# Kernel optimization log

Measured on AMD Instinct MI355X. Metric: run time of the kernel, lower is better.

## Reference

```python
import jax, jax.numpy as jnp
import numpy as np

BITWIDTH = 8
SCALE = 2.0 ** (BITWIDTH - 1)  # bipolar SC quantization levels


def quantize(v):
    """SourceGen/BSGen over 2^bitwidth cycles converges to the bitwidth-quantized
    bipolar value in [-1, 1]; straight-through estimator keeps grads alive."""
    q = jnp.round(jnp.clip(v, -1.0, 1.0) * SCALE) / SCALE
    return v + jax.lax.stop_gradient(q - v)


def sc_clip(v):
    # non-scaled SC accumulation saturates the bipolar range [-1, 1]
    return jnp.clip(v, -1.0, 1.0)


def fsu_relu(v):
    # FSUReLU on bipolar streams: negative rates -> 0, stays in [0, 1]
    return jnp.clip(v, 0.0, 1.0)


def conv2d(x, w):
    # NCHW conv, padding=1, stride=1 (HUBConv2d / FSUConv2d rate-level math)
    return jax.lax.conv_general_dilated(
        x, w, window_strides=(1, 1), padding=[(1, 1), (1, 1)],
        dimension_numbers=("NCHW", "OIHW", "NCHW"))


def setup_inputs() -> dict:
    key = jax.random.key(0)
    ks = jax.random.split(key, 8)
    B, W, H, Wd = 2048, 10, 10, 11
    cnn_chn, fc_sz, hid, n_cls = 16, 256, 64, 7
    fc3_in = H * Wd * cnn_chn * 2  # 3520
    s = 0.1
    return {
        "x": jax.random.normal(ks[0], (B, W, H, Wd), jnp.float32) * 0.5,
        "conv1_w": jax.random.normal(ks[1], (cnn_chn, 1, 3, 3), jnp.float32) * s,
        "conv2_w": jax.random.normal(ks[2], (cnn_chn * 2, cnn_chn, 3, 3), jnp.float32) * s,
        "fc3_w": jax.random.normal(ks[3], (fc_sz, fc3_in), jnp.float32) * s,
        "w_ih": jax.random.normal(ks[4], (2 * hid, fc_sz), jnp.float32) * s,
        "w_hh": jax.random.normal(ks[5], (2 * hid, hid), jnp.float32) * s,
        "fc5_w": jax.random.normal(ks[6], (n_cls, hid), jnp.float32) * s,
    }


def _forward(x, conv1_w, conv2_w, fc3_w, w_ih, w_hh, fc5_w):
    B = x.shape[0]
    hid = w_hh.shape[1]

    def mgu_cell(x_t, hx):
        # FSUMGUCell, hard nonlinearities (rnn_hard=True)
        gi = x_t @ w_ih.T                         # [B, 2H]
        gh = hx @ w_hh.T                          # [B, 2H]
        gi_f, gi_n = jnp.split(gi, 2, axis=-1)
        gh_f, gh_n = jnp.split(gh, 2, axis=-1)
        forgetgate = jnp.clip(0.5 * (gi_f + gh_f) + 0.5, 0.0, 1.0)  # hard sigmoid
        newgate_prod = forgetgate * gh_n
        newgate = jnp.clip(gi_n + newgate_prod, -1.0, 1.0)          # hard tanh
        forgetgate_inv_prod = (1.0 - forgetgate) * newgate
        forgetgate_prod = forgetgate * hx
        return forgetgate_inv_prod + forgetgate_prod

    def step(hx, x_win):
        xi = quantize(x_win)[:, None, :, :]        # [B,1,10,11] bitstream rate
        a1 = fsu_relu(sc_clip(conv2d(xi, conv1_w)))
        a2 = fsu_relu(sc_clip(conv2d(a1, conv2_w)))
        f = a2.reshape(B, -1)                      # [B, 3520]
        a3 = fsu_relu(sc_clip(f @ fc3_w.T))        # [B, 256]
        hq = quantize(hx)
        hx_new = mgu_cell(a3, hq)
        return hx_new, None

    hx0 = jnp.zeros((B, hid), x.dtype)
    xs = jnp.transpose(x, (1, 0, 2, 3))            # [W, B, 10, 11]
    hx, _ = jax.lax.scan(step, hx0, xs)
    return hx @ fc5_w.T                            # [B, 7] fc5 logits


def reference(x, conv1_w, conv2_w, fc3_w, w_ih, w_hh, fc5_w):
    return _forward(x, conv1_w, conv2_w, fc3_w, w_ih, w_hh, fc5_w)
```

## Files before the change

### kernel.cpp

```cpp
#include <hip/hip_runtime.h>
#include <hip/hip_bf16.h>
#include <cstdint>
#include <cstddef>


typedef __bf16 bf16x8v __attribute__((ext_vector_type(8)));
typedef float  f32x4   __attribute__((ext_vector_type(4)));

#define WAVE_FENCE() asm volatile("s_waitcnt lgkmcnt(0)" ::: "memory")

#define A1_PS 24
#define A1_RS (13 * A1_PS)
#define A1_ZS (12 * A1_RS)
#define A1_BS 3776
#define XQ_RS 20
#define XQ_BS 256

#define FC3_K 3584

__global__ __launch_bounds__(256) void cvt_all_k(
    const float* __restrict__ fc3w, const float* __restrict__ w2g,
    const float* __restrict__ wih,  const float* __restrict__ whh,
    __hip_bfloat16* __restrict__ w3p, __hip_bfloat16* __restrict__ w2p,
    __hip_bfloat16* __restrict__ wfi, __hip_bfloat16* __restrict__ wfh)
{
    int bid = blockIdx.x;
    if (bid < 3584) {
        int idx = bid * 256 + threadIdx.x;
        int n = idx / FC3_K, kp = idx % FC3_K;
        int mt = kp >> 9, r = kp & 511;
        int fq = r >> 7, col = (r >> 3) & 15, nt = (r >> 2) & 1, j = r & 3;
        int pixel = mt * 16 + fq * 4 + j, oc = nt * 16 + col;
        float v = (pixel < 110) ? fc3w[n * 3520 + oc * 110 + pixel] : 0.f;
        w3p[idx] = __float2bfloat16(v);
    } else if (bid < 3604) {
        int idx = (bid - 3584) * 256 + threadIdx.x;
        if (idx < 5120) {
            int oc = idx / 160, k = idx % 160;
            int koff = k >> 4, ic = k & 15;
            float v = (koff < 9) ? w2g[(oc * 16 + ic) * 9 + koff] : 0.f;
            w2p[idx] = __float2bfloat16(v);
        }
    } else if (bid < 3860) {
        int idx = (bid - 3604) * 256 + threadIdx.x;
        int e = idx & 7, lane = (idx >> 3) & 63, hl = (idx >> 9) & 1;
        int kt = (idx >> 10) & 7, nt = (idx >> 13) & 7;
        int gate = nt * 16 + (lane & 15);
        int k = kt * 32 + (lane >> 4) * 8 + e;
        float v = wih[gate * 256 + k];
        __hip_bfloat16 hi = __float2bfloat16(v);
        wfi[idx] = hl ? __float2bfloat16(v - __bfloat162float(hi)) : hi;
    } else {
        int idx = (bid - 3860) * 256 + threadIdx.x;
        int e = idx & 7, lane = (idx >> 3) & 63, hl = (idx >> 9) & 1;
        int kt = (idx >> 10) & 1, nt = (idx >> 11) & 7;
        int gate = nt * 16 + (lane & 15);
        int k = kt * 32 + (lane >> 4) * 8 + e;
        float v = whh[gate * 64 + k];
        __hip_bfloat16 hi = __float2bfloat16(v);
        wfh[idx] = hl ? __float2bfloat16(v - __bfloat162float(hi)) : hi;
    }
}

__global__ __launch_bounds__(256) void conv_all_k(
    const float* __restrict__ x, const float* __restrict__ w1g,
    const __hip_bfloat16* __restrict__ w2p,
    __hip_bfloat16* __restrict__ a2p)
{
    __shared__ __hip_bfloat16 a1_s[4 * A1_BS];
    __shared__ float xq_s[4 * XQ_BS];

    const int tid  = threadIdx.x;
    const int wv   = tid >> 6, lane = tid & 63;
    const int t    = blockIdx.x >> 9;
    const int b    = (blockIdx.x & 511) * 4 + wv;
    const int ab   = wv * A1_BS;
    const int xb   = wv * XQ_BS;

    const int fr  = lane & 15, fq = lane >> 4;
    const int fqh = fq >> 1,  icb = (fq & 1) * 8;

    bf16x8v bfrag[5][2];
#pragma unroll
    for (int kt = 0; kt < 5; ++kt)
#pragma unroll
        for (int nt = 0; nt < 2; ++nt)
            bfrag[kt][nt] = *(const bf16x8v*)&w2p[(nt * 16 + fr) * 160 + kt * 32 + fq * 8];

    const int ocp = lane & 7, rs = lane >> 3;
    float w1a[9], w1b[9];
#pragma unroll
    for (int k = 0; k < 9; ++k) {
        w1a[k] = w1g[(2 * ocp) * 9 + k];
        w1b[k] = w1g[(2 * ocp + 1) * 9 + k];
    }

    {
        bf16x8v z = {};
#pragma unroll
        for (int i = 0; i < 8; ++i) {
            int c = lane + i * 64;
            if (c < A1_BS / 8) *(bf16x8v*)&a1_s[ab + c * 8] = z;
        }
        float4 zf = {0.f, 0.f, 0.f, 0.f};
        *(float4*)&xq_s[xb + lane * 4] = zf;
    }
    WAVE_FENCE();

#pragma unroll
    for (int pass = 0; pass < 2; ++pass) {
        int p = pass * 64 + lane;
        if (p < 110) {
            float xv = x[(size_t)b * 1100 + t * 110 + p];
            xv = fminf(fmaxf(xv, -1.f), 1.f);
            xv = rintf(xv * 128.f) * 0.0078125f;
            int h = p / 11, w = p - h * 11;
            xq_s[xb + (h + 1) * XQ_RS + (w + 1)] = xv;
        }
    }
    WAVE_FENCE();

#pragma unroll
    for (int pass = 0; pass < 2; ++pass) {
        const int hr = pass == 0 ? rs : rs + 8;
        if (hr < 10) {
            float acc0[11], acc1[11];
#pragma unroll
            for (int w = 0; w < 11; ++w) { acc0[w] = 0.f; acc1[w] = 0.f; }
#pragma unroll
            for (int dr = 0; dr < 3; ++dr) {
                float xr[16];
                const float* row = &xq_s[xb + (hr + dr) * XQ_RS];
#pragma unroll
                for (int j = 0; j < 4; ++j)
                    *(float4*)&xr[j * 4] = *(const float4*)&row[j * 4];
#pragma unroll
                for (int dc = 0; dc < 3; ++dc) {
                    float wa = w1a[dr * 3 + dc], wb = w1b[dr * 3 + dc];
#pragma unroll
                    for (int w = 0; w < 11; ++w) {
                        acc0[w] += xr[w + dc] * wa;
                        acc1[w] += xr[w + dc] * wb;
                    }
                }
            }
#pragma unroll
            for (int w = 0; w < 11; ++w) {
                __hip_bfloat162 pr;
                pr.x = __float2bfloat16(fminf(fmaxf(acc0[w], 0.f), 1.f));
                pr.y = __float2bfloat16(fminf(fmaxf(acc1[w], 0.f), 1.f));
                *(__hip_bfloat162*)&a1_s[ab + (hr + 1) * A1_RS + (w + 1) * A1_PS + 2 * ocp] = pr;
            }
        }
    }
    WAVE_FENCE();

    const int d0 = fqh * 24 + icb;
    const int d1 = (fqh ? 312 : 48) + icb;
    const int d2 = 336 + fqh * 24 + icb;
    const int d3 = 624 + fqh * 24 + icb;

#pragma unroll
    for (int m = 0; m < 7; ++m) {
        int p = m * 16 + fr; if (p > 109) p = 109;
        int h = p / 11, w = p - h * 11;
        const int bm = ab + h * A1_RS + w * A1_PS;
        f32x4 acc0 = {0.f, 0.f, 0.f, 0.f}, acc1 = {0.f, 0.f, 0.f, 0.f};
        bf16x8v a;
        a = *(const bf16x8v*)&a1_s[bm + d0];
        acc0 = __builtin_amdgcn_mfma_f32_16x16x32_bf16(a, bfrag[0][0], acc0, 0, 0, 0);
        acc1 = __builtin_amdgcn_mfma_f32_16x16x32_bf16(a, bfrag[0][1], acc1, 0, 0, 0);
        a = *(const bf16x8v*)&a1_s[bm + d1];
        acc0 = __builtin_amdgcn_mfma_f32_16x16x32_bf16(a, bfrag[1][0], acc0, 0, 0, 0);
        acc1 = __builtin_amdgcn_mfma_f32_16x16x32_bf16(a, bfrag[1][1], acc1, 0, 0, 0);
        a = *(const bf16x8v*)&a1_s[bm + d2];
        acc0 = __builtin_amdgcn_mfma_f32_16x16x32_bf16(a, bfrag[2][0], acc0, 0, 0, 0);
        acc1 = __builtin_amdgcn_mfma_f32_16x16x32_bf16(a, bfrag[2][1], acc1, 0, 0, 0);
        a = *(const bf16x8v*)&a1_s[bm + d3];
        acc0 = __builtin_amdgcn_mfma_f32_16x16x32_bf16(a, bfrag[3][0], acc0, 0, 0, 0);
        acc1 = __builtin_amdgcn_mfma_f32_16x16x32_bf16(a, bfrag[3][1], acc1, 0, 0, 0);
        a = *(const bf16x8v*)&a1_s[fqh ? (ab + A1_ZS) : (bm + 672 + icb)];
        acc0 = __builtin_amdgcn_mfma_f32_16x16x32_bf16(a, bfrag[4][0], acc0, 0, 0, 0);
        acc1 = __builtin_amdgcn_mfma_f32_16x16x32_bf16(a, bfrag[4][1], acc1, 0, 0, 0);

        bf16x8v ov;
#pragma unroll
        for (int j = 0; j < 4; ++j) {
            bool valid = (m * 16 + fq * 4 + j) < 110;
            float v0 = valid ? fminf(fmaxf(acc0[j], 0.f), 1.f) : 0.f;
            float v1 = valid ? fminf(fmaxf(acc1[j], 0.f), 1.f) : 0.f;
            ov[j]     = (__bf16)v0;
            ov[4 + j] = (__bf16)v1;
        }
        *(bf16x8v*)&a2p[(size_t)(t * 2048 + b) * FC3_K + m * 512 + lane * 8] = ov;
    }
}

__global__ __launch_bounds__(256) void fc3_all_k(
    const __hip_bfloat16* __restrict__ A,
    const __hip_bfloat16* __restrict__ W,
    __hip_bfloat16* __restrict__ a3)
{
    __shared__ __hip_bfloat16 As[3 * 128 * 64];
    __shared__ __hip_bfloat16 Bs[3 * 64 * 64];

    const int tid  = threadIdx.x;
    const int wv   = tid >> 6;
    const int lane = tid & 63;

    const int d    = blockIdx.x;
    const int xcd  = d & 7;
    const int slot = d >> 3;
    const int n0   = (slot & 3) * 64;
    const int m0   = (xcd * 20 + (slot >> 2)) * 128;

    const int wr = wv >> 1, wc = wv & 1;

    const int srow   = lane >> 3;
    const int schunk = lane & 7;
    const int swzc   = schunk ^ srow;

    const int fr = lane & 15;
    const int fq = lane >> 4;

    const __hip_bfloat16* gA0 = A + (size_t)(m0 + wv * 32 +  0 + srow) * FC3_K + swzc * 8;
    const __hip_bfloat16* gA1 = A + (size_t)(m0 + wv * 32 +  8 + srow) * FC3_K + swzc * 8;
    const __hip_bfloat16* gA2 = A + (size_t)(m0 + wv * 32 + 16 + srow) * FC3_K + swzc * 8;
    const __hip_bfloat16* gA3 = A + (size_t)(m0 + wv * 32 + 24 + srow) * FC3_K + swzc * 8;
    const __hip_bfloat16* gB0 = W + (size_t)(n0 + wv * 16 +  0 + srow) * FC3_K + swzc * 8;
    const __hip_bfloat16* gB1 = W + (size_t)(n0 + wv * 16 +  8 + srow) * FC3_K + swzc * 8;

    __hip_bfloat16* ldsA0 = &As[(wv * 32 +  0) * 64];
    __hip_bfloat16* ldsA1 = &As[(wv * 32 +  8) * 64];
    __hip_bfloat16* ldsA2 = &As[(wv * 32 + 16) * 64];
    __hip_bfloat16* ldsA3 = &As[(wv * 32 + 24) * 64];
    __hip_bfloat16* ldsB0 = &Bs[(wv * 16 +  0) * 64];
    __hip_bfloat16* ldsB1 = &Bs[(wv * 16 +  8) * 64];

#define GLD(src, dst, boff)                                                   \
    __builtin_amdgcn_global_load_lds(                                          \
        (const __attribute__((address_space(1))) void*)(src),                  \
        (__attribute__((address_space(3))) void*)((dst) + (boff)), 16, 0, 0)

#define STAGE(b)                                                               \
    do {                                                                       \
        GLD(gA0, ldsA0, (b) * 8192); GLD(gA1, ldsA1, (b) * 8192);              \
        GLD(gA2, ldsA2, (b) * 8192); GLD(gA3, ldsA3, (b) * 8192);              \
        GLD(gB0, ldsB0, (b) * 4096); GLD(gB1, ldsB1, (b) * 4096);              \
        gA0 += 64; gA1 += 64; gA2 += 64; gA3 += 64; gB0 += 64; gB1 += 64;      \
    } while (0)

    int aofs[2][4], bofs[2][2];
#pragma unroll
    for (int kk = 0; kk < 2; ++kk) {
#pragma unroll
        for (int mi = 0; mi < 4; ++mi) {
            const int rr = wr * 64 + mi * 16 + fr;
            aofs[kk][mi] = rr * 64 + (((kk * 4 + fq) ^ (rr & 7)) * 8);
        }
#pragma unroll
        for (int ni = 0; ni < 2; ++ni) {
            const int rr = wc * 32 + ni * 16 + fr;
            bofs[kk][ni] = rr * 64 + (((kk * 4 + fq) ^ (rr & 7)) * 8);
        }
    }

    f32x4 acc[4][2];
#pragma unroll
    for (int mi = 0; mi < 4; ++mi)
#pragma unroll
        for (int ni = 0; ni < 2; ++ni)
            acc[mi][ni] = (f32x4){0.f, 0.f, 0.f, 0.f};

#define COMPUTE(b)                                                             \
    do {                                                                       \
        const __hip_bfloat16* Ab = &As[(b) * 8192];                            \
        const __hip_bfloat16* Bb = &Bs[(b) * 4096];                            \
        _Pragma("unroll")                                                      \
        for (int kk = 0; kk < 2; ++kk) {                                       \
            bf16x8v af[4], bfv[2];                                             \
            _Pragma("unroll")                                                  \
            for (int mi = 0; mi < 4; ++mi)                                     \
                af[mi] = *(const bf16x8v*)&Ab[aofs[kk][mi]];                   \
            _Pragma("unroll")                                                  \
            for (int ni = 0; ni < 2; ++ni)                                     \
                bfv[ni] = *(const bf16x8v*)&Bb[bofs[kk][ni]];                  \
            _Pragma("unroll")                                                  \
            for (int mi = 0; mi < 4; ++mi)                                     \
                _Pragma("unroll")                                              \
                for (int ni = 0; ni < 2; ++ni)                                 \
                    acc[mi][ni] = __builtin_amdgcn_mfma_f32_16x16x32_bf16(     \
                        af[mi], bfv[ni], acc[mi][ni], 0, 0, 0);                \
        }                                                                      \
    } while (0)

#define WAITV(n) asm volatile("s_waitcnt vmcnt(" #n ")" ::: "memory")

    STAGE(0);
    STAGE(1);

    for (int it = 0; it < 18; ++it) {
        WAITV(6); __builtin_amdgcn_s_barrier(); COMPUTE(0); STAGE(2);
        WAITV(6); __builtin_amdgcn_s_barrier(); COMPUTE(1); STAGE(0);
        WAITV(6); __builtin_amdgcn_s_barrier(); COMPUTE(2); STAGE(1);
    }
    WAITV(6); __builtin_amdgcn_s_barrier(); COMPUTE(0);
    WAITV(0); __builtin_amdgcn_s_barrier(); COMPUTE(1);

#undef GLD
#undef STAGE
#undef COMPUTE
#undef WAITV

#pragma unroll
    for (int mi = 0; mi < 4; ++mi)
#pragma unroll
        for (int ni = 0; ni < 2; ++ni)
#pragma unroll
            for (int j = 0; j < 4; ++j) {
                int row = m0 + wr * 64 + mi * 16 + fq * 4 + j;
                int col = n0 + wc * 32 + ni * 16 + fr;
                float v = fminf(fmaxf(acc[mi][ni][j], 0.f), 1.f);
                a3[(size_t)row * 256 + col] = __float2bfloat16(v);
            }
}

__global__ __launch_bounds__(256, 1) void mgu_all_k(
    const __hip_bfloat16* __restrict__ a3,
    const __hip_bfloat16* __restrict__ wfi, const __hip_bfloat16* __restrict__ wfh,
    const float* __restrict__ w5, float* __restrict__ out)
{
    __shared__ __hip_bfloat16 a3_s[16 * 256];
    __shared__ __hip_bfloat16 hq_s[16 * 64];
    __shared__ float hx_s[16 * 64];
    __shared__ float w5_s[7 * 64];

    const int tid = threadIdx.x;
    const int wv  = tid >> 6, lane = tid & 63;
    const int fr  = lane & 15, fq = lane >> 4;
    const int b0  = blockIdx.x * 16;
    const int ntf = wv, ntn = wv + 4;

    bf16x8v wiF[8][2], wiN[8][2], whF[2][2], whN[2][2];
#pragma unroll
    for (int kt = 0; kt < 8; ++kt)
#pragma unroll
        for (int hl = 0; hl < 2; ++hl) {
            wiF[kt][hl] = *(const bf16x8v*)&wfi[(((ntf * 8 + kt) * 2 + hl) * 64 + lane) * 8];
            wiN[kt][hl] = *(const bf16x8v*)&wfi[(((ntn * 8 + kt) * 2 + hl) * 64 + lane) * 8];
        }
#pragma unroll
    for (int kt = 0; kt < 2; ++kt)
#pragma unroll
        for (int hl = 0; hl < 2; ++hl) {
            whF[kt][hl] = *(const bf16x8v*)&wfh[(((ntf * 2 + kt) * 2 + hl) * 64 + lane) * 8];
            whN[kt][hl] = *(const bf16x8v*)&wfh[(((ntn * 2 + kt) * 2 + hl) * 64 + lane) * 8];
        }

    for (int i = tid; i < 16 * 64; i += 256) hx_s[i] = 0.f;
    for (int i = tid; i < 7 * 64; i += 256) w5_s[i] = w5[i];
    __syncthreads();

    for (int t = 0; t < 10; ++t) {
#pragma unroll
        for (int pass = 0; pass < 2; ++pass) {
            int i = pass * 256 + tid;
            int r = i >> 5, cq = i & 31;
            bf16x8v v = *(const bf16x8v*)&a3[((size_t)(t * 2048 + b0 + r)) * 256 + cq * 8];
            *(bf16x8v*)&a3_s[r * 256 + ((cq ^ (r & 7)) * 8)] = v;
        }
#pragma unroll
        for (int pass = 0; pass < 4; ++pass) {
            int i = pass * 256 + tid;
            int r = i >> 6, c = i & 63;
            float v = hx_s[r * 64 + c];
            v = fminf(fmaxf(v, -1.f), 1.f);
            v = rintf(v * 128.f) * 0.0078125f;
            hq_s[r * 64 + (((c >> 3) ^ (r & 7)) << 3) + (c & 7)] = __float2bfloat16(v);
        }
        __syncthreads();

        f32x4 accF  = {0.f, 0.f, 0.f, 0.f};
        f32x4 accNi = {0.f, 0.f, 0.f, 0.f};
        f32x4 accNh = {0.f, 0.f, 0.f, 0.f};
#pragma unroll
        for (int kt = 0; kt < 8; ++kt) {
            bf16x8v a = *(const bf16x8v*)&a3_s[fr * 256 + (((kt * 4 + fq) ^ (fr & 7)) * 8)];
            accF  = __builtin_amdgcn_mfma_f32_16x16x32_bf16(a, wiF[kt][0], accF, 0, 0, 0);
            accF  = __builtin_amdgcn_mfma_f32_16x16x32_bf16(a, wiF[kt][1], accF, 0, 0, 0);
            accNi = __builtin_amdgcn_mfma_f32_16x16x32_bf16(a, wiN[kt][0], accNi, 0, 0, 0);
            accNi = __builtin_amdgcn_mfma_f32_16x16x32_bf16(a, wiN[kt][1], accNi, 0, 0, 0);
        }
#pragma unroll
        for (int kt = 0; kt < 2; ++kt) {
            bf16x8v a = *(const bf16x8v*)&hq_s[fr * 64 + (((kt * 4 + fq) ^ (fr & 7)) * 8)];
            accF  = __builtin_amdgcn_mfma_f32_16x16x32_bf16(a, whF[kt][0], accF, 0, 0, 0);
            accF  = __builtin_amdgcn_mfma_f32_16x16x32_bf16(a, whF[kt][1], accF, 0, 0, 0);
            accNh = __builtin_amdgcn_mfma_f32_16x16x32_bf16(a, whN[kt][0], accNh, 0, 0, 0);
            accNh = __builtin_amdgcn_mfma_f32_16x16x32_bf16(a, whN[kt][1], accNh, 0, 0, 0);
        }

        const int j5 = wv * 16 + fr;
#pragma unroll
        for (int j = 0; j < 4; ++j) {
            int b = fq * 4 + j;
            float f = fminf(fmaxf(0.5f * accF[j] + 0.5f, 0.f), 1.f);
            float n = fminf(fmaxf(accNi[j] + f * accNh[j], -1.f), 1.f);
            float hq = __bfloat162float(
                hq_s[b * 64 + ((((j5) >> 3) ^ (b & 7)) << 3) + (j5 & 7)]);
            hx_s[b * 64 + j5] = (1.f - f) * n + f * hq;
        }
        __syncthreads();
    }

    if (tid < 112) {
        int b = tid / 7, c = tid % 7;
        float acc = 0.f;
#pragma unroll
        for (int k = 0; k < 64; ++k) acc += hx_s[b * 64 + k] * w5_s[c * 64 + k];
        out[(size_t)(b0 + b) * 7 + c] = acc;
    }
}

extern "C" void kernel_launch(void* const* d_in, const int* in_sizes, int n_in,
                              void* d_out, int out_size, void* d_ws, size_t ws_size,
                              hipStream_t stream)
{
    const float* x    = (const float*)d_in[0];
    const float* w1   = (const float*)d_in[1];
    const float* w2   = (const float*)d_in[2];
    const float* fc3w = (const float*)d_in[3];
    const float* wih  = (const float*)d_in[4];
    const float* whh  = (const float*)d_in[5];
    const float* fc5w = (const float*)d_in[6];
    float* out = (float*)d_out;

    char* ws = (char*)d_ws;
    __hip_bfloat16* a2p = (__hip_bfloat16*)ws;
    __hip_bfloat16* a3  = (__hip_bfloat16*)(ws + 146800640);
    __hip_bfloat16* w3p = (__hip_bfloat16*)(ws + 157286400);
    __hip_bfloat16* w2p = (__hip_bfloat16*)(ws + 159121408);
    __hip_bfloat16* wfi = (__hip_bfloat16*)(ws + 159131648);
    __hip_bfloat16* wfh = (__hip_bfloat16*)(ws + 159262720);

    cvt_all_k<<<3924, 256, 0, stream>>>(fc3w, w2, wih, whh, w3p, w2p, wfi, wfh);
    conv_all_k<<<5120, 256, 0, stream>>>(x, w1, w2p, a2p);
    fc3_all_k<<<640, 256, 0, stream>>>(a2p, w3p, a3);
    mgu_all_k<<<128, 256, 0, stream>>>(a3, wfi, wfh, fc5w, out);
}
```

Measured before the change: 121.9 us.

## Restructure fc3 GEMM into single-wave 64x64 tiles without block barriers

The fc3 GEMM moves from 4-wave blocks computing 128x64 tiles with a triple-buffered LDS pipeline to 1-wave blocks computing 64x64 tiles with double buffering. Because each block is a single wave, the s_barrier calls are gone and only vmcnt waits guard the async global-to-LDS loads. s_setprio is also raised around the MFMA bursts. The aim is to cut barrier stalls and raise MFMA work per wave. In exchange the grid holds half as many waves and each block reuses less data than a 128x64 tile, so latency hiding and L2 traffic may suffer.

```diff
diff --git a/kernel.cpp b/kernel.cpp
--- a/kernel.cpp
+++ b/kernel.cpp
@@ -8,6 +8,7 @@
 typedef float  f32x4   __attribute__((ext_vector_type(4)));
 
 #define WAVE_FENCE() asm volatile("s_waitcnt lgkmcnt(0)" ::: "memory")
+#define WAITV(n) asm volatile("s_waitcnt vmcnt(" #n ")" ::: "memory")
 
 #define A1_PS 24
 #define A1_RS (13 * A1_PS)
@@ -196,25 +197,21 @@
     }
 }
 
-__global__ __launch_bounds__(256) void fc3_all_k(
+__global__ __launch_bounds__(64) void fc3_all_k(
     const __hip_bfloat16* __restrict__ A,
     const __hip_bfloat16* __restrict__ W,
     __hip_bfloat16* __restrict__ a3)
 {
-    __shared__ __hip_bfloat16 As[3 * 128 * 64];
-    __shared__ __hip_bfloat16 Bs[3 * 64 * 64];
-
-    const int tid  = threadIdx.x;
-    const int wv   = tid >> 6;
-    const int lane = tid & 63;
+    __shared__ __hip_bfloat16 As[2 * 64 * 64];
+    __shared__ __hip_bfloat16 Bs[2 * 64 * 64];
+
+    const int lane = threadIdx.x;
 
     const int d    = blockIdx.x;
     const int xcd  = d & 7;
     const int slot = d >> 3;
     const int n0   = (slot & 3) * 64;
-    const int m0   = (xcd * 20 + (slot >> 2)) * 128;
-
-    const int wr = wv >> 1, wc = wv & 1;
+    const int m0   = (xcd * 40 + (slot >> 2)) * 64;
 
     const int srow   = lane >> 3;
     const int schunk = lane & 7;
@@ -223,19 +220,22 @@
     const int fr = lane & 15;
     const int fq = lane >> 4;
 
-    const __hip_bfloat16* gA0 = A + (size_t)(m0 + wv * 32 +  0 + srow) * FC3_K + swzc * 8;
-    const __hip_bfloat16* gA1 = A + (size_t)(m0 + wv * 32 +  8 + srow) * FC3_K + swzc * 8;
-    const __hip_bfloat16* gA2 = A + (size_t)(m0 + wv * 32 + 16 + srow) * FC3_K + swzc * 8;
-    const __hip_bfloat16* gA3 = A + (size_t)(m0 + wv * 32 + 24 + srow) * FC3_K + swzc * 8;
-    const __hip_bfloat16* gB0 = W + (size_t)(n0 + wv * 16 +  0 + srow) * FC3_K + swzc * 8;
-    const __hip_bfloat16* gB1 = W + (size_t)(n0 + wv * 16 +  8 + srow) * FC3_K + swzc * 8;
-
-    __hip_bfloat16* ldsA0 = &As[(wv * 32 +  0) * 64];
-    __hip_bfloat16* ldsA1 = &As[(wv * 32 +  8) * 64];
-    __hip_bfloat16* ldsA2 = &As[(wv * 32 + 16) * 64];
-    __hip_bfloat16* ldsA3 = &As[(wv * 32 + 24) * 64];
-    __hip_bfloat16* ldsB0 = &Bs[(wv * 16 +  0) * 64];
-    __hip_bfloat16* ldsB1 = &Bs[(wv * 16 +  8) * 64];
+    const __hip_bfloat16* gA0 = A + (size_t)(m0 +  0 + srow) * FC3_K + swzc * 8;
+    const __hip_bfloat16* gA1 = A + (size_t)(m0 +  8 + srow) * FC3_K + swzc * 8;
+    const __hip_bfloat16* gA2 = A + (size_t)(m0 + 16 + srow) * FC3_K + swzc * 8;
+    const __hip_bfloat16* gA3 = A + (size_t)(m0 + 24 + srow) * FC3_K + swzc * 8;
+    const __hip_bfloat16* gA4 = A + (size_t)(m0 + 32 + srow) * FC3_K + swzc * 8;
+    const __hip_bfloat16* gA5 = A + (size_t)(m0 + 40 + srow) * FC3_K + swzc * 8;
+    const __hip_bfloat16* gA6 = A + (size_t)(m0 + 48 + srow) * FC3_K + swzc * 8;
+    const __hip_bfloat16* gA7 = A + (size_t)(m0 + 56 + srow) * FC3_K + swzc * 8;
+    const __hip_bfloat16* gB0 = W + (size_t)(n0 +  0 + srow) * FC3_K + swzc * 8;
+    const __hip_bfloat16* gB1 = W + (size_t)(n0 +  8 + srow) * FC3_K + swzc * 8;
+    const __hip_bfloat16* gB2 = W + (size_t)(n0 + 16 + srow) * FC3_K + swzc * 8;
+    const __hip_bfloat16* gB3 = W + (size_t)(n0 + 24 + srow) * FC3_K + swzc * 8;
+    const __hip_bfloat16* gB4 = W + (size_t)(n0 + 32 + srow) * FC3_K + swzc * 8;
+    const __hip_bfloat16* gB5 = W + (size_t)(n0 + 40 + srow) * FC3_K + swzc * 8;
+    const __hip_bfloat16* gB6 = W + (size_t)(n0 + 48 + srow) * FC3_K + swzc * 8;
+    const __hip_bfloat16* gB7 = W + (size_t)(n0 + 56 + srow) * FC3_K + swzc * 8;
 
 #define GLD(src, dst, boff)                                                   \
     __builtin_amdgcn_global_load_lds(                                          \
@@ -244,82 +244,81 @@
 
 #define STAGE(b)                                                               \
     do {                                                                       \
-        GLD(gA0, ldsA0, (b) * 8192); GLD(gA1, ldsA1, (b) * 8192);              \
-        GLD(gA2, ldsA2, (b) * 8192); GLD(gA3, ldsA3, (b) * 8192);              \
-        GLD(gB0, ldsB0, (b) * 4096); GLD(gB1, ldsB1, (b) * 4096);              \
-        gA0 += 64; gA1 += 64; gA2 += 64; gA3 += 64; gB0 += 64; gB1 += 64;      \
+        GLD(gA0, As, (b) * 4096 +    0); GLD(gA1, As, (b) * 4096 +  512);      \
+        GLD(gA2, As, (b) * 4096 + 1024); GLD(gA3, As, (b) * 4096 + 1536);      \
+        GLD(gA4, As, (b) * 4096 + 2048); GLD(gA5, As, (b) * 4096 + 2560);      \
+        GLD(gA6, As, (b) * 4096 + 3072); GLD(gA7, As, (b) * 4096 + 3584);      \
+        GLD(gB0, Bs, (b) * 4096 +    0); GLD(gB1, Bs, (b) * 4096 +  512);      \
+        GLD(gB2, Bs, (b) * 4096 + 1024); GLD(gB3, Bs, (b) * 4096 + 1536);      \
+        GLD(gB4, Bs, (b) * 4096 + 2048); GLD(gB5, Bs, (b) * 4096 + 2560);      \
+        GLD(gB6, Bs, (b) * 4096 + 3072); GLD(gB7, Bs, (b) * 4096 + 3584);      \
+        gA0 += 64; gA1 += 64; gA2 += 64; gA3 += 64;                            \
+        gA4 += 64; gA5 += 64; gA6 += 64; gA7 += 64;                            \
+        gB0 += 64; gB1 += 64; gB2 += 64; gB3 += 64;                            \
+        gB4 += 64; gB5 += 64; gB6 += 64; gB7 += 64;                            \
     } while (0)
 
-    int aofs[2][4], bofs[2][2];
-#pragma unroll
-    for (int kk = 0; kk < 2; ++kk) {
-#pragma unroll
-        for (int mi = 0; mi < 4; ++mi) {
-            const int rr = wr * 64 + mi * 16 + fr;
-            aofs[kk][mi] = rr * 64 + (((kk * 4 + fq) ^ (rr & 7)) * 8);
-        }
-#pragma unroll
-        for (int ni = 0; ni < 2; ++ni) {
-            const int rr = wc * 32 + ni * 16 + fr;
-            bofs[kk][ni] = rr * 64 + (((kk * 4 + fq) ^ (rr & 7)) * 8);
-        }
-    }
-
-    f32x4 acc[4][2];
+    int tofs[2][4];
+#pragma unroll
+    for (int kk = 0; kk < 2; ++kk)
+#pragma unroll
+        for (int i = 0; i < 4; ++i) {
+            const int rr = i * 16 + fr;
+            tofs[kk][i] = rr * 64 + (((kk * 4 + fq) ^ (rr & 7)) * 8);
+        }
+
+    f32x4 acc[4][4];
 #pragma unroll
     for (int mi = 0; mi < 4; ++mi)
 #pragma unroll
-        for (int ni = 0; ni < 2; ++ni)
+        for (int ni = 0; ni < 4; ++ni)
             acc[mi][ni] = (f32x4){0.f, 0.f, 0.f, 0.f};
 
 #define COMPUTE(b)                                                             \
     do {                                                                       \
-        const __hip_bfloat16* Ab = &As[(b) * 8192];                            \
+        const __hip_bfloat16* Ab = &As[(b) * 4096];                            \
         const __hip_bfloat16* Bb = &Bs[(b) * 4096];                            \
         _Pragma("unroll")                                                      \
         for (int kk = 0; kk < 2; ++kk) {                                       \
-            bf16x8v af[4], bfv[2];                                             \
+            bf16x8v af[4], bfv[4];                                             \
             _Pragma("unroll")                                                  \
-            for (int mi = 0; mi < 4; ++mi)                                     \
-                af[mi] = *(const bf16x8v*)&Ab[aofs[kk][mi]];                   \
-            _Pragma("unroll")                                                  \
-            for (int ni = 0; ni < 2; ++ni)                                     \
-                bfv[ni] = *(const bf16x8v*)&Bb[bofs[kk][ni]];                  \
+            for (int i = 0; i < 4; ++i) {                                      \
+                af[i]  = *(const bf16x8v*)&Ab[tofs[kk][i]];                    \
+                bfv[i] = *(const bf16x8v*)&Bb[tofs[kk][i]];                    \
+            }                                                                  \
+            __builtin_amdgcn_s_setprio(1);                                     \
             _Pragma("unroll")                                                  \
             for (int mi = 0; mi < 4; ++mi)                                     \
                 _Pragma("unroll")                                              \
-                for (int ni = 0; ni < 2; ++ni)                                 \
+                for (int ni = 0; ni < 4; ++ni)                                 \
                     acc[mi][ni] = __builtin_amdgcn_mfma_f32_16x16x32_bf16(     \
                         af[mi], bfv[ni], acc[mi][ni], 0, 0, 0);                \
+            __builtin_amdgcn_s_setprio(0);                                     \
         }                                                                      \
     } while (0)
 
-#define WAITV(n) asm volatile("s_waitcnt vmcnt(" #n ")" ::: "memory")
-
     STAGE(0);
     STAGE(1);
 
-    for (int it = 0; it < 18; ++it) {
-        WAITV(6); __builtin_amdgcn_s_barrier(); COMPUTE(0); STAGE(2);
-        WAITV(6); __builtin_amdgcn_s_barrier(); COMPUTE(1); STAGE(0);
-        WAITV(6); __builtin_amdgcn_s_barrier(); COMPUTE(2); STAGE(1);
-    }
-    WAITV(6); __builtin_amdgcn_s_barrier(); COMPUTE(0);
-    WAITV(0); __builtin_amdgcn_s_barrier(); COMPUTE(1);
+    for (int it = 0; it < 27; ++it) {
+        WAITV(16); COMPUTE(0); STAGE(0);
+        WAITV(16); COMPUTE(1); STAGE(1);
+    }
+    WAITV(16); COMPUTE(0);
+    WAITV(0);  COMPUTE(1);
 
 #undef GLD
 #undef STAGE
 #undef COMPUTE
-#undef WAITV
 
 #pragma unroll
     for (int mi = 0; mi < 4; ++mi)
 #pragma unroll
-        for (int ni = 0; ni < 2; ++ni)
+        for (int ni = 0; ni < 4; ++ni)
 #pragma unroll
             for (int j = 0; j < 4; ++j) {
-                int row = m0 + wr * 64 + mi * 16 + fq * 4 + j;
-                int col = n0 + wc * 32 + ni * 16 + fr;
+                int row = m0 + mi * 16 + fq * 4 + j;
+                int col = n0 + ni * 16 + fr;
                 float v = fminf(fmaxf(acc[mi][ni][j], 0.f), 1.f);
                 a3[(size_t)row * 256 + col] = __float2bfloat16(v);
             }
@@ -445,6 +444,6 @@
 
     cvt_all_k<<<3924, 256, 0, stream>>>(fc3w, w2, wih, whh, w3p, w2p, wfi, wfh);
     conv_all_k<<<5120, 256, 0, stream>>>(x, w1, w2p, a2p);
-    fc3_all_k<<<640, 256, 0, stream>>>(a2p, w3p, a3);
+    fc3_all_k<<<1280, 64, 0, stream>>>(a2p, w3p, a3);
     mgu_all_k<<<128, 256, 0, stream>>>(a3, wfi, wfh, fc5w, out);
 }
```

Result: slower. 135.4 us (+11.1%).
